# Kernel tuning notes

Measured on AMD Instinct MI355X. Metric: run time of the kernel, lower is better.

Reference implementation:

```python
import jax, jax.numpy as jnp
import numpy as np

DIM = 768
NUM_HEADS = 12
HEAD_DIM = DIM // NUM_HEADS
SCALE = HEAD_DIM ** -0.5


def setup_inputs() -> dict:
    key = jax.random.key(0)
    ks = jax.random.split(key, 6)
    B, N, C = 4, 2048, DIM
    x = jax.random.normal(ks[0], (B, N, C), dtype=jnp.float32)
    qkv_weight = jax.random.normal(ks[1], (3 * C, C), dtype=jnp.float32) * (C ** -0.5)
    q_bias = jax.random.normal(ks[2], (C,), dtype=jnp.float32) * 0.02
    v_bias = jax.random.normal(ks[3], (C,), dtype=jnp.float32) * 0.02
    proj_weight = jax.random.normal(ks[4], (C, C), dtype=jnp.float32) * (C ** -0.5)
    proj_bias = jax.random.normal(ks[5], (C,), dtype=jnp.float32) * 0.02
    return {"x": x, "qkv_weight": qkv_weight, "q_bias": q_bias,
            "v_bias": v_bias, "proj_weight": proj_weight, "proj_bias": proj_bias}


def reference(x, qkv_weight, q_bias, v_bias, proj_weight, proj_bias):
    B, N, C = x.shape
    # bias = concat(q_bias, zeros_like(v_bias), v_bias)
    bias = jnp.concatenate([q_bias, jnp.zeros_like(v_bias), v_bias])
    qkv = x @ qkv_weight.T + bias                      # [B, N, 3C]
    qkv = qkv.reshape(B, N, 3, NUM_HEADS, HEAD_DIM)
    q, k, v = jnp.moveaxis(qkv, 2, 0)                  # each [B, N, H, hd]
    q = jnp.transpose(q, (0, 2, 1, 3)) * SCALE         # [B, H, N, hd]
    k = jnp.transpose(k, (0, 2, 1, 3))
    v = jnp.transpose(v, (0, 2, 1, 3))
    attn = jax.nn.softmax(jnp.einsum('bhqd,bhkd->bhqk', q, k), axis=-1)
    out = jnp.einsum('bhqk,bhkd->bhqd', attn, v)       # [B, H, N, hd]
    out = jnp.transpose(out, (0, 2, 1, 3)).reshape(B, N, C)
    return out @ proj_weight.T + proj_bias
```

## Files before the change

### kernel.cpp

```cpp
#include <hip/hip_runtime.h>
#include <cstdint>
#include <cstddef>

typedef _Float16 f16;
typedef _Float16 f16x8 __attribute__((ext_vector_type(8)));
typedef _Float16 f16x4 __attribute__((ext_vector_type(4)));
typedef __fp16 h16x2 __attribute__((ext_vector_type(2)));
typedef float f32x4 __attribute__((ext_vector_type(4)));
typedef float f32x16 __attribute__((ext_vector_type(16)));

#define DIM 768
#define NHEAD 12
#define HD 64
#define BATCH 4
#define SEQ 2048
#define MROWS (BATCH*SEQ)
#define C3 (3*DIM)
#define NBH (BATCH*NHEAD)

__device__ __forceinline__ f32x4 mfma32(f16x8 a, f16x8 b, f32x4 c) {
  return __builtin_amdgcn_mfma_f32_16x16x32_f16(a, b, c, 0, 0, 0);
}
__device__ __forceinline__ f32x16 mfma3232(f16x8 a, f16x8 b, f32x16 c) {
  return __builtin_amdgcn_mfma_f32_32x32x16_f16(a, b, c, 0, 0, 0);
}

__device__ __forceinline__ void gl2lds16(const void* g, void* l) {
  __builtin_amdgcn_global_load_lds(
      (const __attribute__((address_space(1))) void*)g,
      (__attribute__((address_space(3))) void*)l, 16, 0, 0);
}

__global__ __launch_bounds__(256) void k_convert(
    const float* __restrict__ x, const float* __restrict__ wqkv,
    const float* __restrict__ wproj,
    f16* __restrict__ xh, f16* __restrict__ wqh, f16* __restrict__ wph)
{
  const int NX = MROWS*DIM/4, NW = C3*DIM/4;
  int i = blockIdx.x * 256 + threadIdx.x;
  const float4* src; f16* dst; int idx;
  if (i < NX)         { src = (const float4*)x;     dst = xh;  idx = i; }
  else if (i < NX+NW) { src = (const float4*)wqkv;  dst = wqh; idx = i - NX; }
  else                { src = (const float4*)wproj; dst = wph; idx = i - NX - NW; }
  float4 v = src[idx];
  union { f16 h[4]; uint64_t u; } r;
  r.h[0] = (f16)v.x; r.h[1] = (f16)v.y; r.h[2] = (f16)v.z; r.h[3] = (f16)v.w;
  ((uint64_t*)dst)[idx] = r.u;
}

__device__ __forceinline__ void gemm_tile(
    const f16* __restrict__ A, const f16* __restrict__ B,
    int lda, int ldb, int K, int am0, int bn0,
    f16* smem, f32x4 acc[4][4])
{
  f16* sA0 = smem;         f16* sA1 = smem + 4096;
  f16* sB0 = smem + 8192;  f16* sB1 = smem + 12288;
  const int tid = threadIdx.x, wid = tid >> 6;
  const int lane = tid & 63, lane15 = lane & 15, quad = lane >> 4;
  const int wm = wid >> 1, wn = wid & 1;

  auto stage = [&](int k0, f16* sA, f16* sB) {
    #pragma unroll
    for (int i = 0; i < 2; i++) {
      int j = i*256 + tid;
      int row = j >> 2;
      int sc  = (j & 3) ^ ((row >> 1) & 3);
      gl2lds16(A + (size_t)(am0 + row)*lda + k0 + sc*8, sA + (i*256 + wid*64)*8);
      gl2lds16(B + (size_t)(bn0 + row)*ldb + k0 + sc*8, sB + (i*256 + wid*64)*8);
    }
  };

  const int NK = K >> 5;
  stage(0, sA0, sB0);
  for (int kk = 0; kk < NK; kk++) {
    f16* cA = (kk & 1) ? sA1 : sA0;
    f16* cB = (kk & 1) ? sB1 : sB0;
    __syncthreads();
    if (kk + 1 < NK)
      stage((kk + 1) << 5, (kk & 1) ? sA0 : sA1, (kk & 1) ? sB0 : sB1);
    f16x8 af[4], bf[4];
    #pragma unroll
    for (int t = 0; t < 4; t++) {
      int ra = wm*64 + t*16 + lane15;
      af[t] = *(const f16x8*)(cA + ra*32 + ((quad ^ ((ra >> 1) & 3)) << 3));
      int rb = wn*64 + t*16 + lane15;
      bf[t] = *(const f16x8*)(cB + rb*32 + ((quad ^ ((rb >> 1) & 3)) << 3));
    }
    #pragma unroll
    for (int mt = 0; mt < 4; mt++)
      #pragma unroll
      for (int nt = 0; nt < 4; nt++)
        acc[mt][nt] = mfma32(af[mt], bf[nt], acc[mt][nt]);
  }
}

__device__ __forceinline__ void gemm_tile512(
    const f16* __restrict__ A, const f16* __restrict__ B,
    int lda, int ldb, int K, int am0, int bn0,
    f16* smem, f32x4 acc[4][2])
{
  f16* sA0 = smem;         f16* sA1 = smem + 4096;
  f16* sB0 = smem + 8192;  f16* sB1 = smem + 12288;
  const int tid = threadIdx.x, wid = tid >> 6;
  const int lane = tid & 63, lane15 = lane & 15, quad = lane >> 4;
  const int wm = wid >> 2, wn = wid & 3;

  auto stage = [&](int k0, f16* sA, f16* sB) {
    int row = tid >> 2;
    int sc  = (tid & 3) ^ ((row >> 1) & 3);
    gl2lds16(A + (size_t)(am0 + row)*lda + k0 + sc*8, sA + (wid*64)*8);
    gl2lds16(B + (size_t)(bn0 + row)*ldb + k0 + sc*8, sB + (wid*64)*8);
  };

  const int NK = K >> 5;
  stage(0, sA0, sB0);
  for (int kk = 0; kk < NK; kk++) {
    f16* cA = (kk & 1) ? sA1 : sA0;
    f16* cB = (kk & 1) ? sB1 : sB0;
    __syncthreads();
    if (kk + 1 < NK)
      stage((kk + 1) << 5, (kk & 1) ? sA0 : sA1, (kk & 1) ? sB0 : sB1);
    f16x8 af[4], bf[2];
    #pragma unroll
    for (int t = 0; t < 4; t++) {
      int ra = wm*64 + t*16 + lane15;
      af[t] = *(const f16x8*)(cA + ra*32 + ((quad ^ ((ra >> 1) & 3)) << 3));
    }
    #pragma unroll
    for (int t = 0; t < 2; t++) {
      int rb = wn*32 + t*16 + lane15;
      bf[t] = *(const f16x8*)(cB + rb*32 + ((quad ^ ((rb >> 1) & 3)) << 3));
    }
    #pragma unroll
    for (int mt = 0; mt < 4; mt++)
      #pragma unroll
      for (int nt = 0; nt < 2; nt++)
        acc[mt][nt] = mfma32(af[mt], bf[nt], acc[mt][nt]);
  }
}

__global__ __launch_bounds__(256, 4) void k_qkv(
    const f16* __restrict__ xh, const f16* __restrict__ wqh,
    const float* __restrict__ q_bias, const float* __restrict__ v_bias,
    f16* __restrict__ Qh, f16* __restrict__ Kh, f16* __restrict__ Vt)
{
  __shared__ f16 smem[16384];
  f32x4 acc[4][4];
  const f32x4 z4 = {0.f, 0.f, 0.f, 0.f};
  #pragma unroll
  for (int a = 0; a < 4; a++)
    #pragma unroll
    for (int b = 0; b < 4; b++) acc[a][b] = z4;

  const int tid = threadIdx.x, wid = tid >> 6, lane = tid & 63;
  const int lane15 = lane & 15, quad = lane >> 4;
  const int wm = wid >> 1, wn = wid & 1;
  const int cblk = blockIdx.x * 128;
  const int mblk = blockIdx.y * 128;
  const int bb = mblk >> 11, nbase = mblk & (SEQ - 1);
  const float QS = 0.125f * 1.4426950408889634f;

  if (cblk < 2*DIM) {
    gemm_tile(wqh, xh, DIM, DIM, DIM, cblk, mblk, smem, acc);
    const bool isQ = (cblk < DIM);
    #pragma unroll
    for (int mt = 0; mt < 4; mt++) {
      int c0 = cblk + wm*64 + mt*16 + quad*4;
      int cr = isQ ? c0 : (c0 - DIM);
      int h = cr >> 6, d0 = cr & 63;
      float4 qb4 = isQ ? *(const float4*)(q_bias + c0) : make_float4(0,0,0,0);
      f16* dst = isQ ? Qh : Kh;
      f16* base = dst + (((size_t)(bb*NHEAD + h)*SEQ + nbase) << 6) + d0;
      #pragma unroll
      for (int nt = 0; nt < 4; nt++) {
        int n = wn*64 + nt*16 + lane15;
        f32x4 v = acc[mt][nt];
        f16x4 hv;
        if (isQ) {
          hv[0] = (f16)((v[0] + qb4.x) * QS); hv[1] = (f16)((v[1] + qb4.y) * QS);
          hv[2] = (f16)((v[2] + qb4.z) * QS); hv[3] = (f16)((v[3] + qb4.w) * QS);
        } else {
          hv[0] = (f16)v[0]; hv[1] = (f16)v[1]; hv[2] = (f16)v[2]; hv[3] = (f16)v[3];
        }
        *(f16x4*)(base + ((size_t)n << 6)) = hv;
      }
    }
  } else {
    gemm_tile(xh, wqh, DIM, DIM, DIM, mblk, cblk, smem, acc);
    #pragma unroll
    for (int nt = 0; nt < 4; nt++) {
      int c = cblk + wn*64 + nt*16 + lane15;
      int c2 = c - 2*DIM;
      int h = c2 >> 6, d = c2 & 63;
      float b = v_bias[c2];
      f16* base = Vt + ((size_t)(bb*NHEAD + h)*HD + d)*SEQ + nbase;
      #pragma unroll
      for (int mt = 0; mt < 4; mt++) {
        int n0 = wm*64 + mt*16 + quad*4;
        f32x4 v = acc[mt][nt];
        f16x4 hv = {(f16)(v[0]+b), (f16)(v[1]+b), (f16)(v[2]+b), (f16)(v[3]+b)};
        *(f16x4*)(base + n0) = hv;
      }
    }
  }
}

#define KVT 128
#define NIT (SEQ/KVT)
__global__ __launch_bounds__(256, 3) void k_attn(
    const f16* __restrict__ Qh, const f16* __restrict__ Kh,
    const f16* __restrict__ Vt, f16* __restrict__ attnh)
{
  __shared__ f16 smem[2*8192 + 64*132];
  f16* sK0 = smem;
  f16* sK1 = smem + 8192;
  f16* sV  = smem + 16384;

  const int tid = threadIdx.x, wid = tid >> 6, lane = tid & 63;
  const int l31 = lane & 31, hi = lane >> 5;

  const int L = blockIdx.x;
  const int xcd = L & 7, kk = L >> 3;
  const int bh = xcd + 8*(kk >> 4);
  const int q0 = (kk & 15) * 128;
  const int qw = q0 + wid*32;

  const f16* Kbh = Kh + (size_t)bh*SEQ*HD;
  const f16* Vbh = Vt + (size_t)bh*HD*SEQ;

  f16x8 qf[4];
  #pragma unroll
  for (int ks = 0; ks < 4; ks++)
    qf[ks] = *(const f16x8*)(Qh + ((size_t)bh*SEQ + qw + l31)*HD + ks*16 + hi*8);

  const f32x16 z16 = {0.f,0.f,0.f,0.f, 0.f,0.f,0.f,0.f,
                      0.f,0.f,0.f,0.f, 0.f,0.f,0.f,0.f};
  f32x16 o0 = z16, o1 = z16, sacc = z16;
  f16x8 one8;
  #pragma unroll
  for (int j = 0; j < 8; j++) one8[j] = (f16)1.f;

  auto stageK = [&](int kv0, f16* sK) {
    #pragma unroll
    for (int i = 0; i < 4; i++) {
      int j = i*256 + tid;
      int row = j >> 3;
      int sc  = (j & 7) ^ (row & 7);
      gl2lds16(Kbh + (size_t)(kv0 + row)*HD + sc*8, sK + (i*256 + wid*64)*8);
    }
  };

  int koff[4];
  #pragma unroll
  for (int ks = 0; ks < 4; ks++)
    koff[ks] = l31*64 + (((2*ks + hi) ^ (l31 & 7)) << 3);

  const int vrow = tid >> 2, vcg = (tid & 3) * 32;
  const f16* vsrc = Vbh + (size_t)vrow*SEQ + vcg;

  stageK(0, sK0);
  f16x8 vreg[4];
  #pragma unroll
  for (int j = 0; j < 4; j++) vreg[j] = *(const f16x8*)(vsrc + j*8);

#define ASTEP(SCUR, SNXT, CC, HASNXT)                                         \
  do {                                                                        \
    const int vo = (CC)*32 + 4*hi;                                            \
    union { f16x4 q[2]; f16x8 v; } a00, a01, a10, a11;                        \
    a00.q[0] = *(const f16x4*)(sV + l31*132 + vo);                            \
    a00.q[1] = *(const f16x4*)(sV + l31*132 + vo + 8);                        \
    a01.q[0] = *(const f16x4*)(sV + l31*132 + vo + 16);                       \
    a01.q[1] = *(const f16x4*)(sV + l31*132 + vo + 24);                       \
    a10.q[0] = *(const f16x4*)(sV + (32 + l31)*132 + vo);                     \
    a10.q[1] = *(const f16x4*)(sV + (32 + l31)*132 + vo + 8);                 \
    a11.q[0] = *(const f16x4*)(sV + (32 + l31)*132 + vo + 16);                \
    a11.q[1] = *(const f16x4*)(sV + (32 + l31)*132 + vo + 24);                \
    unsigned hx[8];                                                           \
    _Pragma("unroll")                                                         \
    for (int r = 0; r < 8; r++) {                                             \
      union { h16x2 p2; unsigned u; } uu;                                     \
      uu.p2 = __builtin_amdgcn_cvt_pkrtz(                                     \
          __builtin_amdgcn_exp2f((SCUR)[2*r]),                                \
          __builtin_amdgcn_exp2f((SCUR)[2*r+1]));                             \
      hx[r] = uu.u;                                                           \
    }                                                                         \
    union { unsigned w[4]; f16x8 v; } b0u, b1u;                               \
    b0u.w[0]=hx[0]; b0u.w[1]=hx[1]; b0u.w[2]=hx[2]; b0u.w[3]=hx[3];           \
    b1u.w[0]=hx[4]; b1u.w[1]=hx[5]; b1u.w[2]=hx[6]; b1u.w[3]=hx[7];           \
    if (HASNXT) {                                                             \
      (SNXT) = z16;                                                           \
      __builtin_amdgcn_s_setprio(1);                                          \
      _Pragma("unroll")                                                       \
      for (int ks = 0; ks < 4; ks++) {                                        \
        f16x8 ka = *(const f16x8*)(cK + ((CC)+1)*2048 + koff[ks]);            \
        (SNXT) = mfma3232(ka, qf[ks], (SNXT));                                \
      }                                                                       \
      __builtin_amdgcn_s_setprio(0);                                          \
    }                                                                         \
    __builtin_amdgcn_s_setprio(1);                                            \
    sacc = mfma3232(one8, b0u.v, sacc);                                       \
    o0 = mfma3232(a00.v, b0u.v, o0);                                          \
    o1 = mfma3232(a10.v, b0u.v, o1);                                          \
    sacc = mfma3232(one8, b1u.v, sacc);                                       \
    o0 = mfma3232(a01.v, b1u.v, o0);                                          \
    o1 = mfma3232(a11.v, b1u.v, o1);                                          \
    __builtin_amdgcn_s_setprio(0);                                            \
  } while (0)

  for (int it = 0; it < NIT; it++) {
    f16* cK = (it & 1) ? sK1 : sK0;
    __syncthreads();
    #pragma unroll
    for (int j = 0; j < 4; j++) {
      union { f16x8 v; f16x4 h[2]; } u; u.v = vreg[j];
      *(f16x4*)(sV + vrow*132 + vcg + j*8)     = u.h[0];
      *(f16x4*)(sV + vrow*132 + vcg + j*8 + 4) = u.h[1];
    }
    __syncthreads();
    if (it + 1 < NIT) {
      stageK((it + 1)*KVT, (it & 1) ? sK0 : sK1);
      #pragma unroll
      for (int j = 0; j < 4; j++)
        vreg[j] = *(const f16x8*)(vsrc + (it + 1)*KVT + j*8);
    }

    f32x16 s0, s1;
    s0 = z16;
    __builtin_amdgcn_s_setprio(1);
    #pragma unroll
    for (int ks = 0; ks < 4; ks++) {
      f16x8 ka = *(const f16x8*)(cK + koff[ks]);
      s0 = mfma3232(ka, qf[ks], s0);
    }
    __builtin_amdgcn_s_setprio(0);
    ASTEP(s0, s1, 0, 1);
    ASTEP(s1, s0, 1, 1);
    ASTEP(s0, s1, 2, 1);
    ASTEP(s1, s0, 3, 0);
  }
#undef ASTEP

  const float inv = 1.f / sacc[0];

  __syncthreads();
  f16* tb = smem + wid * (32 * 72);
  #pragma unroll
  for (int g = 0; g < 4; g++) {
    f16x4 h0v = {(f16)(o0[4*g+0]*inv), (f16)(o0[4*g+1]*inv),
                 (f16)(o0[4*g+2]*inv), (f16)(o0[4*g+3]*inv)};
    *(f16x4*)(tb + l31*72 + g*8 + hi*4) = h0v;
    f16x4 h1v = {(f16)(o1[4*g+0]*inv), (f16)(o1[4*g+1]*inv),
                 (f16)(o1[4*g+2]*inv), (f16)(o1[4*g+3]*inv)};
    *(f16x4*)(tb + l31*72 + 32 + g*8 + hi*4) = h1v;
  }
  __syncthreads();
  const int b = bh / NHEAD, hh = bh % NHEAD;
  #pragma unroll
  for (int i = 0; i < 4; i++) {
    int row = i*8 + (lane >> 3);
    f16x8 rv = *(const f16x8*)(tb + row*72 + (lane & 7)*8);
    *(f16x8*)(attnh + ((size_t)b*SEQ + qw + row)*DIM + hh*HD + (lane & 7)*8) = rv;
  }
}

__global__ __launch_bounds__(512, 4) void k_proj(
    const f16* __restrict__ ah, const f16* __restrict__ wph,
    const float* __restrict__ pbias, float* __restrict__ out)
{
  __shared__ f16 smem[16384];
  f32x4 acc[4][2];
  const f32x4 z4 = {0.f, 0.f, 0.f, 0.f};
  #pragma unroll
  for (int a = 0; a < 4; a++)
    #pragma unroll
    for (int b = 0; b < 2; b++) acc[a][b] = z4;

  const int cblk = blockIdx.y * 128;
  const int mblk = blockIdx.x * 128;
  gemm_tile512(wph, ah, DIM, DIM, DIM, cblk, mblk, smem, acc);

  const int tid = threadIdx.x, wid = tid >> 6, lane = tid & 63;
  const int lane15 = lane & 15, quad = lane >> 4;
  const int wm = wid >> 2, wn = wid & 3;
  #pragma unroll
  for (int mt = 0; mt < 4; mt++) {
    int c0 = cblk + wm*64 + mt*16 + quad*4;
    float4 b4 = *(const float4*)(pbias + c0);
    #pragma unroll
    for (int nt = 0; nt < 2; nt++) {
      int m = mblk + wn*32 + nt*16 + lane15;
      f32x4 v = acc[mt][nt];
      float4 r = make_float4(v[0]+b4.x, v[1]+b4.y, v[2]+b4.z, v[3]+b4.w);
      *(float4*)(out + (size_t)m*DIM + c0) = r;
    }
  }
}

extern "C" void kernel_launch(void* const* d_in, const int* in_sizes, int n_in,
                              void* d_out, int out_size, void* d_ws, size_t ws_size,
                              hipStream_t stream) {
  const float* x    = (const float*)d_in[0];
  const float* wqkv = (const float*)d_in[1];
  const float* qb   = (const float*)d_in[2];
  const float* vb   = (const float*)d_in[3];
  const float* wp   = (const float*)d_in[4];
  const float* pb   = (const float*)d_in[5];
  float* out = (float*)d_out;

  f16* p = (f16*)d_ws;
  f16* xh  = p; p += (size_t)MROWS*DIM;
  f16* wqh = p; p += (size_t)C3*DIM;
  f16* wph = p; p += (size_t)DIM*DIM;
  f16* Qh  = p; p += (size_t)NBH*SEQ*HD;
  f16* Kh  = p; p += (size_t)NBH*SEQ*HD;
  f16* Vt  = p; p += (size_t)NBH*SEQ*HD;
  f16* attnh = xh;

  k_convert<<<8448, 256, 0, stream>>>(x, wqkv, wp, xh, wqh, wph);
  k_qkv<<<dim3(C3/128, MROWS/128), 256, 0, stream>>>(xh, wqh, qb, vb, Qh, Kh, Vt);
  k_attn<<<dim3((SEQ/128)*NBH), 256, 0, stream>>>(Qh, Kh, Vt, attnh);
  k_proj<<<dim3(MROWS/128, DIM/128), 512, 0, stream>>>(attnh, wph, pb, out);
}
```

Baseline: 220.4 us.

## Enlarge QKV GEMM tiles to 128x256 with 512 threads; merge softmax row-sum MFMAs

```diff
diff --git a/kernel.cpp b/kernel.cpp
--- a/kernel.cpp
+++ b/kernel.cpp
@@ -48,25 +48,31 @@
   ((uint64_t*)dst)[idx] = r.u;
 }
 
-__device__ __forceinline__ void gemm_tile(
+template<int RA, int RB, int WN>
+__device__ __forceinline__ void gemm_tile512b(
     const f16* __restrict__ A, const f16* __restrict__ B,
     int lda, int ldb, int K, int am0, int bn0,
     f16* smem, f32x4 acc[4][4])
 {
-  f16* sA0 = smem;         f16* sA1 = smem + 4096;
-  f16* sB0 = smem + 8192;  f16* sB1 = smem + 12288;
-  const int tid = threadIdx.x, wid = tid >> 6;
+  const int ASZ = RA*32, BSZ = RB*32;
+  f16* sA0 = smem;            f16* sA1 = smem + ASZ;
+  f16* sB0 = smem + 2*ASZ;    f16* sB1 = smem + 2*ASZ + BSZ;
+  const int tid = threadIdx.x;
   const int lane = tid & 63, lane15 = lane & 15, quad = lane >> 4;
-  const int wm = wid >> 1, wn = wid & 1;
+  const int wid = tid >> 6;
+  const int wm = wid / WN, wn = wid % WN;
 
   auto stage = [&](int k0, f16* sA, f16* sB) {
     #pragma unroll
-    for (int i = 0; i < 2; i++) {
-      int j = i*256 + tid;
+    for (int i = 0; i < 3; i++) {
+      int j = i*512 + tid;
       int row = j >> 2;
       int sc  = (j & 3) ^ ((row >> 1) & 3);
-      gl2lds16(A + (size_t)(am0 + row)*lda + k0 + sc*8, sA + (i*256 + wid*64)*8);
-      gl2lds16(B + (size_t)(bn0 + row)*ldb + k0 + sc*8, sB + (i*256 + wid*64)*8);
+      if (row < RA)
+        gl2lds16(A + (size_t)(am0 + row)*lda + k0 + sc*8, sA + j*8);
+      else
+        gl2lds16(B + (size_t)(bn0 + row - RA)*ldb + k0 + sc*8,
+                 sB + (j - RA*4)*8);
     }
   };
 
@@ -139,12 +145,12 @@
   }
 }
 
-__global__ __launch_bounds__(256, 4) void k_qkv(
+__global__ __launch_bounds__(512, 4) void k_qkv(
     const f16* __restrict__ xh, const f16* __restrict__ wqh,
     const float* __restrict__ q_bias, const float* __restrict__ v_bias,
     f16* __restrict__ Qh, f16* __restrict__ Kh, f16* __restrict__ Vt)
 {
-  __shared__ f16 smem[16384];
+  __shared__ f16 smem[24576];
   f32x4 acc[4][4];
   const f32x4 z4 = {0.f, 0.f, 0.f, 0.f};
   #pragma unroll
@@ -154,14 +160,15 @@
 
   const int tid = threadIdx.x, wid = tid >> 6, lane = tid & 63;
   const int lane15 = lane & 15, quad = lane >> 4;
-  const int wm = wid >> 1, wn = wid & 1;
-  const int cblk = blockIdx.x * 128;
-  const int mblk = blockIdx.y * 128;
-  const int bb = mblk >> 11, nbase = mblk & (SEQ - 1);
   const float QS = 0.125f * 1.4426950408889634f;
-
-  if (cblk < 2*DIM) {
-    gemm_tile(wqh, xh, DIM, DIM, DIM, cblk, mblk, smem, acc);
+  const int bx = blockIdx.x;
+
+  if (bx < 384) {
+    const int cblk = (bx % 12) * 128;
+    const int mblk = (bx / 12) * 256;
+    const int bb = mblk >> 11, nbase = mblk & (SEQ - 1);
+    gemm_tile512b<128, 256, 4>(wqh, xh, DIM, DIM, DIM, cblk, mblk, smem, acc);
+    const int wm = wid >> 2, wn = wid & 3;
     const bool isQ = (cblk < DIM);
     #pragma unroll
     for (int mt = 0; mt < 4; mt++) {
@@ -186,7 +193,12 @@
       }
     }
   } else {
-    gemm_tile(xh, wqh, DIM, DIM, DIM, mblk, cblk, smem, acc);
+    const int b2 = bx - 384;
+    const int cblk = 2*DIM + (b2 % 6) * 128;
+    const int mblk = (b2 / 6) * 256;
+    const int bb = mblk >> 11, nbase = mblk & (SEQ - 1);
+    gemm_tile512b<256, 128, 2>(xh, wqh, DIM, DIM, DIM, mblk, cblk, smem, acc);
+    const int wm = wid >> 1, wn = wid & 1;
     #pragma unroll
     for (int nt = 0; nt < 4; nt++) {
       int c = cblk + wn*64 + nt*16 + lane15;
@@ -297,11 +309,11 @@
       }                                                                       \
       __builtin_amdgcn_s_setprio(0);                                          \
     }                                                                         \
+    f16x8 bsum = b0u.v + b1u.v;               \
     __builtin_amdgcn_s_setprio(1);                                            \
-    sacc = mfma3232(one8, b0u.v, sacc);                                       \
+    sacc = mfma3232(one8, bsum, sacc);                                        \
     o0 = mfma3232(a00.v, b0u.v, o0);                                          \
     o1 = mfma3232(a10.v, b0u.v, o1);                                          \
-    sacc = mfma3232(one8, b1u.v, sacc);                                       \
     o0 = mfma3232(a01.v, b1u.v, o0);                                          \
     o1 = mfma3232(a11.v, b1u.v, o1);                                          \
     __builtin_amdgcn_s_setprio(0);                                            \
@@ -417,7 +429,7 @@
   f16* attnh = xh;
 
   k_convert<<<8448, 256, 0, stream>>>(x, wqkv, wp, xh, wqh, wph);
-  k_qkv<<<dim3(C3/128, MROWS/128), 256, 0, stream>>>(xh, wqh, qb, vb, Qh, Kh, Vt);
+  k_qkv<<<576, 512, 0, stream>>>(xh, wqh, qb, vb, Qh, Kh, Vt);
   k_attn<<<dim3((SEQ/128)*NBH), 256, 0, stream>>>(Qh, Kh, Vt, attnh);
   k_proj<<<dim3(MROWS/128, DIM/128), 512, 0, stream>>>(attnh, wph, pb, out);
 }
```

New measurement: 228.9 us. +3.9%, slower.
